# Performance work log

Measured on AMD Instinct MI355X. Metric: run time of the kernel, lower is better.

The kernel has to match this reference:

```python
import jax, jax.numpy as jnp
import numpy as np

N_NODES = 50000
IN_CH = 256
Z_DIM = 64
N_EDGES = 800000


def setup_inputs() -> dict:
    key = jax.random.key(0)
    k_x, k_e, k_wm, k_ws = jax.random.split(key, 4)
    x = jax.random.normal(k_x, (N_NODES, IN_CH), dtype=jnp.float32)
    edge_index = jax.random.randint(k_e, (2, N_EDGES), 0, N_NODES, dtype=jnp.int64)
    # Glorot-style init like PyG GCNConv
    scale = 1.0 / np.sqrt(IN_CH)
    W_mu = jax.random.uniform(k_wm, (IN_CH, Z_DIM), dtype=jnp.float32, minval=-scale, maxval=scale)
    W_logstd = jax.random.uniform(k_ws, (IN_CH, Z_DIM), dtype=jnp.float32, minval=-scale, maxval=scale)
    b_mu = jnp.zeros((Z_DIM,), dtype=jnp.float32)
    b_logstd = jnp.zeros((Z_DIM,), dtype=jnp.float32)
    return {"x": x, "edge_index": edge_index, "W_mu": W_mu, "b_mu": b_mu,
            "W_logstd": W_logstd, "b_logstd": b_logstd}


def _gcn_conv(x, W, b, src, dst, deg_inv_sqrt, num_nodes):
    # PyG GCNConv: out = D^{-1/2} (A + I) D^{-1/2} X W + b
    xw = x @ W                                   # [N, Z]
    norm = deg_inv_sqrt[src] * deg_inv_sqrt[dst]  # [E+N]
    msg = xw[src] * norm[:, None]                 # gather + scale, [E+N, Z]
    agg = jax.ops.segment_sum(msg, dst, num_segments=num_nodes)  # scatter-add
    return agg + b


def reference(x, edge_index, W_mu, b_mu, W_logstd, b_logstd):
    num_nodes = x.shape[0]
    loops = jnp.arange(num_nodes, dtype=edge_index.dtype)
    src = jnp.concatenate([edge_index[0], loops])
    dst = jnp.concatenate([edge_index[1], loops])
    # degree (with self loops) on target nodes, symmetric normalization
    deg = jax.ops.segment_sum(jnp.ones_like(dst, dtype=x.dtype), dst, num_segments=num_nodes)
    deg_inv_sqrt = jnp.where(deg > 0, jax.lax.rsqrt(jnp.maximum(deg, 1.0)), 0.0)
    mu = _gcn_conv(x, W_mu, b_mu, src, dst, deg_inv_sqrt, num_nodes)
    logstd = _gcn_conv(x, W_logstd, b_logstd, src, dst, deg_inv_sqrt, num_nodes)
    return (mu, logstd)
```

## Files before the change

kernel.cpp:

```cpp
#include <hip/hip_runtime.h>

#define N_NODES 50000
#define IN_CH   256
#define Z_DIM   64
#define N_EDGES 800000
#define CH2     128
#define NODE_OFF (N_NODES * Z_DIM)
#define NBLK    ((N_NODES + 255) / 256)
#define SEG     8
#define SEGN    50048
#define NBUCKET (SEG * SEGN)
#define CAP     16
#define CAPN    64
#define ECHUNKS (N_EDGES / 256)
#define TM      128
#define GTILES  ((N_NODES + TM - 1) / TM)
#define NW      32768

typedef __bf16 bf16x8 __attribute__((ext_vector_type(8)));
typedef float  f32x4  __attribute__((ext_vector_type(4)));

__device__ __forceinline__ unsigned short f2bf(float f) {
    __bf16 h = (__bf16)f;
    unsigned short u;
    __builtin_memcpy(&u, &h, 2);
    return u;
}
__device__ __forceinline__ float bf_lo(unsigned w) { return __uint_as_float(w << 16); }
__device__ __forceinline__ float bf_hi(unsigned w) { return __uint_as_float(w & 0xFFFF0000u); }

__global__ void k_pre(int* __restrict__ cur8,
                      const float* __restrict__ Wmu, const float* __restrict__ Wls,
                      unsigned short* __restrict__ WbT) {
    int g = blockIdx.x * 256 + threadIdx.x;
    if (g < NBUCKET) cur8[g] = 0;
    int h = g - NBUCKET;
    if (h >= 0 && h < NW) {
        int n = h >> 8, k = h & 255;
        float v = (n < 64) ? Wmu[(size_t)k * 64 + n] : Wls[(size_t)k * 64 + (n - 64)];
        WbT[(size_t)n * 256 + k] = f2bf(v);
    }
}

__global__ __launch_bounds__(256) void k_scat(const int* __restrict__ src,
                                              const int* __restrict__ dst,
                                              int* __restrict__ cur8,
                                              unsigned short* __restrict__ pk2) {
    int e = blockIdx.x * 256 + threadIdx.x;
    int s = src[e];
    int d = dst[e];
    unsigned xcc;
    asm("s_getreg_b32 %0, hwreg(HW_REG_XCC_ID)" : "=s"(xcc));
    int idx = (int)(xcc & (SEG - 1)) * SEGN + d;
    int pos = __hip_atomic_fetch_add(&cur8[idx], 1, __ATOMIC_RELAXED,
                                     __HIP_MEMORY_SCOPE_WORKGROUP);
    if (pos < CAP) pk2[(size_t)idx * CAP + pos] = (unsigned short)s;
}

#define CSP2 136
__global__ __launch_bounds__(256, 2) void k_gemm(const float* __restrict__ x,
                                                 const unsigned short* __restrict__ WbT,
                                                 unsigned short* __restrict__ xwb) {
    __shared__ __align__(16) unsigned short As[TM * 256];
    const int tid = threadIdx.x;
    const int r0  = blockIdx.x * TM;

    {
        int row_l0 = tid >> 3;
        int cb     = (tid & 7) * 32;
#pragma unroll
        for (int r = 0; r < 4; ++r) {
            int row_l = r * 32 + row_l0;
            int row   = r0 + row_l;
            char* dpb = (char*)As + row_l * 512;
            unsigned cswz = (unsigned)((row_l & 7) << 4);
            if (row < N_NODES) {
                const float4* xp = (const float4*)(x + (size_t)row * IN_CH + cb);
#pragma unroll
                for (int i = 0; i < 4; ++i) {
                    float4 a = xp[2 * i];
                    float4 b = xp[2 * i + 1];
                    uint4 w;
                    w.x = (unsigned)f2bf(a.x) | ((unsigned)f2bf(a.y) << 16);
                    w.y = (unsigned)f2bf(a.z) | ((unsigned)f2bf(a.w) << 16);
                    w.z = (unsigned)f2bf(b.x) | ((unsigned)f2bf(b.y) << 16);
                    w.w = (unsigned)f2bf(b.z) | ((unsigned)f2bf(b.w) << 16);
                    *(uint4*)(dpb + (((unsigned)(cb * 2 + i * 16)) ^ cswz)) = w;
                }
            } else {
                uint4 z = make_uint4(0, 0, 0, 0);
#pragma unroll
                for (int i = 0; i < 4; ++i)
                    *(uint4*)(dpb + (((unsigned)(cb * 2 + i * 16)) ^ cswz)) = z;
            }
        }
    }
    __syncthreads();

    const int wv    = tid >> 6;
    const int lane  = tid & 63;
    const int m     = lane & 15;
    const int q     = lane >> 4;
    const int rbase = wv * 32;

    f32x4 acc[2][8] = {};
    const char* apb0 = (const char*)As + (rbase + m) * 512;
    const char* apb1 = apb0 + 16 * 512;
    const unsigned   sw  = (unsigned)((m & 7) << 4);
    const unsigned short* bp = WbT + (size_t)m * 256 + q * 8;

#pragma unroll
    for (int k0 = 0; k0 < IN_CH; k0 += 32) {
        unsigned off = ((unsigned)(q * 16 + 2 * k0)) ^ sw;
        bf16x8 a0 = *(const bf16x8*)(apb0 + off);
        bf16x8 a1 = *(const bf16x8*)(apb1 + off);
#pragma unroll
        for (int nt = 0; nt < 8; ++nt) {
            bf16x8 bf_ = *(const bf16x8*)(bp + (size_t)nt * 16 * 256 + k0);
            acc[0][nt] = __builtin_amdgcn_mfma_f32_16x16x32_bf16(a0, bf_, acc[0][nt], 0, 0, 0);
            acc[1][nt] = __builtin_amdgcn_mfma_f32_16x16x32_bf16(a1, bf_, acc[1][nt], 0, 0, 0);
        }
    }

    __syncthreads();
    {
        unsigned short* Css = As;
#pragma unroll
        for (int mi = 0; mi < 2; ++mi)
#pragma unroll
            for (int nt = 0; nt < 8; ++nt)
#pragma unroll
                for (int r = 0; r < 4; ++r)
                    Css[(rbase + mi * 16 + q * 4 + r) * CSP2 + nt * 16 + m] =
                        f2bf(acc[mi][nt][r]);
    }
    __syncthreads();
    {
        int row_l = tid >> 2;
        int c0    = (tid & 3) * 32;
#pragma unroll
        for (int rr = 0; rr < 2; ++rr) {
            int rl  = rr * 64 + row_l;
            int row = r0 + rl;
            if (row < N_NODES) {
                const uint4* cp = (const uint4*)(As + rl * CSP2 + c0);
                uint4 w0 = cp[0];
                uint4 w1 = cp[1];
                uint4 w2 = cp[2];
                uint4 w3 = cp[3];
                uint4* op = (uint4*)(xwb + (size_t)row * CH2 + c0);
                op[0] = w0; op[1] = w1; op[2] = w2; op[3] = w3;
            }
        }
    }
}

__global__ void k_dinv(const int* __restrict__ cur8,
                       const unsigned short* __restrict__ pk2,
                       float* __restrict__ dinv,
                       unsigned short* __restrict__ plist,
                       unsigned short* __restrict__ degc) {
    int i = blockIdx.x * 256 + threadIdx.x;
    if (i >= N_NODES) return;
    int traw = 1;
    int c[SEG];
#pragma unroll
    for (int s = 0; s < SEG; ++s) {
        int cs = cur8[s * SEGN + i];
        traw += cs;
        c[s] = (cs > CAP) ? CAP : cs;
    }
    dinv[i] = rsqrtf((float)traw);

    unsigned short* dp = plist + (size_t)i * CAPN;
    int off = 0;
#pragma unroll
    for (int s = 0; s < SEG; ++s) {
        const unsigned short* sp = pk2 + ((size_t)(s * SEGN + i)) * CAP;
        int cc = c[s];
        int lim = CAPN - off;
        if (cc > lim) cc = lim;
        for (int j = 0; j < cc; ++j) dp[off + j] = sp[j];
        off += cc;
    }
    degc[i] = (unsigned short)off;
}

__global__ __launch_bounds__(256) void k_gather(const unsigned short* __restrict__ plist,
                                                const unsigned short* __restrict__ degc,
                                                const unsigned short* __restrict__ xwb,
                                                const float* __restrict__ dinv,
                                                const float* __restrict__ bmu,
                                                const float* __restrict__ bls,
                                                float* __restrict__ out) {
    const int i  = blockIdx.x * 16 + (threadIdx.x >> 4);
    const int cl = threadIdx.x & 15;

    const float di  = dinv[i];
    const int   deg = degc[i];

    float acc[8];
    {
        float sq = di * di;
        uint4 w = *(const uint4*)(xwb + (size_t)i * CH2 + cl * 8);
        acc[0] = bf_lo(w.x) * sq; acc[1] = bf_hi(w.x) * sq;
        acc[2] = bf_lo(w.y) * sq; acc[3] = bf_hi(w.y) * sq;
        acc[4] = bf_lo(w.z) * sq; acc[5] = bf_hi(w.z) * sq;
        acc[6] = bf_lo(w.w) * sq; acc[7] = bf_hi(w.w) * sq;
    }

    const unsigned short* lp = plist + (size_t)i * CAPN;
    for (int j = 0; j < deg; j += 4) {
        uint2 pe = *(const uint2*)(lp + j);
        int s0 = (int)(pe.x & 0xFFFFu);
        int s1 = (int)(pe.x >> 16);
        int s2 = (int)(pe.y & 0xFFFFu);
        int s3 = (int)(pe.y >> 16);
        int rem = deg - j;
        int e1 = (rem > 1) ? s1 : s0;
        int e2 = (rem > 2) ? s2 : s0;
        int e3 = (rem > 3) ? s3 : s0;
        float n0 = di * dinv[s0];
        float n1 = (rem > 1) ? di * dinv[e1] : 0.f;
        float n2 = (rem > 2) ? di * dinv[e2] : 0.f;
        float n3 = (rem > 3) ? di * dinv[e3] : 0.f;
        const uint4 w0 = *(const uint4*)(xwb + (size_t)s0 * CH2 + cl * 8);
        const uint4 w1 = *(const uint4*)(xwb + (size_t)e1 * CH2 + cl * 8);
        const uint4 w2 = *(const uint4*)(xwb + (size_t)e2 * CH2 + cl * 8);
        const uint4 w3 = *(const uint4*)(xwb + (size_t)e3 * CH2 + cl * 8);
        acc[0] += bf_lo(w0.x) * n0 + bf_lo(w1.x) * n1 + bf_lo(w2.x) * n2 + bf_lo(w3.x) * n3;
        acc[1] += bf_hi(w0.x) * n0 + bf_hi(w1.x) * n1 + bf_hi(w2.x) * n2 + bf_hi(w3.x) * n3;
        acc[2] += bf_lo(w0.y) * n0 + bf_lo(w1.y) * n1 + bf_lo(w2.y) * n2 + bf_lo(w3.y) * n3;
        acc[3] += bf_hi(w0.y) * n0 + bf_hi(w1.y) * n1 + bf_hi(w2.y) * n2 + bf_hi(w3.y) * n3;
        acc[4] += bf_lo(w0.z) * n0 + bf_lo(w1.z) * n1 + bf_lo(w2.z) * n2 + bf_lo(w3.z) * n3;
        acc[5] += bf_hi(w0.z) * n0 + bf_hi(w1.z) * n1 + bf_hi(w2.z) * n2 + bf_hi(w3.z) * n3;
        acc[6] += bf_lo(w0.w) * n0 + bf_lo(w1.w) * n1 + bf_lo(w2.w) * n2 + bf_lo(w3.w) * n3;
        acc[7] += bf_hi(w0.w) * n0 + bf_hi(w1.w) * n1 + bf_hi(w2.w) * n2 + bf_hi(w3.w) * n3;
    }

    {
        int c0 = cl * 8;
        const float* bb = (c0 < 64) ? (bmu + c0) : (bls + (c0 - 64));
        float4 b0 = *(const float4*)(bb + 0);
        float4 b1 = *(const float4*)(bb + 4);
        float* o = (c0 < 64) ? (out + (size_t)i * 64 + c0)
                             : (out + NODE_OFF + (size_t)i * 64 + (c0 - 64));
        *(float4*)(o + 0) = make_float4(acc[0] + b0.x, acc[1] + b0.y,
                                        acc[2] + b0.z, acc[3] + b0.w);
        *(float4*)(o + 4) = make_float4(acc[4] + b1.x, acc[5] + b1.y,
                                        acc[6] + b1.z, acc[7] + b1.w);
    }
}

extern "C" void kernel_launch(void* const* d_in, const int* in_sizes, int n_in,
                              void* d_out, int out_size, void* d_ws, size_t ws_size,
                              hipStream_t stream) {
    const float* x   = (const float*)d_in[0];
    const int*   ei  = (const int*)d_in[1];
    const float* Wmu = (const float*)d_in[2];
    const float* bmu = (const float*)d_in[3];
    const float* Wls = (const float*)d_in[4];
    const float* bls = (const float*)d_in[5];
    float* out = (float*)d_out;

    const int* src = ei;
    const int* dst = ei + N_EDGES;

    char* ws = (char*)d_ws;
    int*            cur8  = (int*)(ws + 0);
    float*          dinv  = (float*)(ws + 1638400);
    unsigned short* WbT   = (unsigned short*)(ws + 1867776);
    unsigned short* pk2   = (unsigned short*)(ws + 2097152);
    unsigned short* xwb   = (unsigned short*)(ws + 16777216);
    unsigned short* plist = (unsigned short*)(ws + 29577216);
    unsigned short* degc  = (unsigned short*)(ws + 35977216);

    k_pre<<<(NBUCKET + NW + 255) / 256, 256, 0, stream>>>(cur8, Wmu, Wls, WbT);
    k_scat<<<ECHUNKS, 256, 0, stream>>>(src, dst, cur8, pk2);
    k_gemm<<<GTILES, 256, 0, stream>>>(x, WbT, xwb);
    k_dinv<<<NBLK, 256, 0, stream>>>(cur8, pk2, dinv, plist, degc);
    k_gather<<<N_NODES / 16, 256, 0, stream>>>(plist, degc, xwb, dinv, bmu, bls, out);
}
```

Before: 204.5 us.

## Parallelize per-node bucket compaction across 8 lanes and bucket scatter by block

The degree/compaction kernel now assigns eight lanes per node, one per segment bucket, and uses a segmented shuffle prefix-sum to compute output offsets, so the serial copy of up to 64 entries per thread becomes parallel copies with better coalescing. The edge scatter stops reading the XCC id register and picks the segment from blockIdx instead, switching to device-scope atomicAdd. This is meant to remove the long serial per-thread loop in compaction. In exchange, the atomics now use a wider scope and the blockIdx-based segment no longer tracks the physical die, which may add cross-die atomic contention.

```diff
diff --git a/kernel.cpp b/kernel.cpp
--- a/kernel.cpp
+++ b/kernel.cpp
@@ -6,7 +6,6 @@
 #define N_EDGES 800000
 #define CH2     128
 #define NODE_OFF (N_NODES * Z_DIM)
-#define NBLK    ((N_NODES + 255) / 256)
 #define SEG     8
 #define SEGN    50048
 #define NBUCKET (SEG * SEGN)
@@ -15,6 +14,7 @@
 #define ECHUNKS (N_EDGES / 256)
 #define TM      128
 #define GTILES  ((N_NODES + TM - 1) / TM)
+#define DBLK    ((N_NODES + 31) / 32)
 #define NW      32768
 
 typedef __bf16 bf16x8 __attribute__((ext_vector_type(8)));
@@ -49,11 +49,8 @@
     int e = blockIdx.x * 256 + threadIdx.x;
     int s = src[e];
     int d = dst[e];
-    unsigned xcc;
-    asm("s_getreg_b32 %0, hwreg(HW_REG_XCC_ID)" : "=s"(xcc));
-    int idx = (int)(xcc & (SEG - 1)) * SEGN + d;
-    int pos = __hip_atomic_fetch_add(&cur8[idx], 1, __ATOMIC_RELAXED,
-                                     __HIP_MEMORY_SCOPE_WORKGROUP);
+    int idx = (blockIdx.x & (SEG - 1)) * SEGN + d;
+    int pos = atomicAdd(&cur8[idx], 1);
     if (pos < CAP) pk2[(size_t)idx * CAP + pos] = (unsigned short)s;
 }
 
@@ -155,35 +152,43 @@
     }
 }
 
-__global__ void k_dinv(const int* __restrict__ cur8,
-                       const unsigned short* __restrict__ pk2,
-                       float* __restrict__ dinv,
-                       unsigned short* __restrict__ plist,
-                       unsigned short* __restrict__ degc) {
-    int i = blockIdx.x * 256 + threadIdx.x;
+__global__ __launch_bounds__(256) void k_dinv(const int* __restrict__ cur8,
+                                              const unsigned short* __restrict__ pk2,
+                                              float* __restrict__ dinv,
+                                              unsigned short* __restrict__ plist,
+                                              unsigned short* __restrict__ degc) {
+    const int i = blockIdx.x * 32 + (threadIdx.x >> 3);
+    const int s = threadIdx.x & 7;
     if (i >= N_NODES) return;
-    int traw = 1;
-    int c[SEG];
-#pragma unroll
-    for (int s = 0; s < SEG; ++s) {
-        int cs = cur8[s * SEGN + i];
-        traw += cs;
-        c[s] = (cs > CAP) ? CAP : cs;
-    }
-    dinv[i] = rsqrtf((float)traw);
-
-    unsigned short* dp = plist + (size_t)i * CAPN;
-    int off = 0;
-#pragma unroll
-    for (int s = 0; s < SEG; ++s) {
-        const unsigned short* sp = pk2 + ((size_t)(s * SEGN + i)) * CAP;
-        int cc = c[s];
-        int lim = CAPN - off;
-        if (cc > lim) cc = lim;
-        for (int j = 0; j < cc; ++j) dp[off + j] = sp[j];
-        off += cc;
-    }
-    degc[i] = (unsigned short)off;
+
+    int cnt = cur8[s * SEGN + i];
+    int cc  = (cnt > CAP) ? CAP : cnt;
+
+    int run = cc;
+#pragma unroll
+    for (int k = 1; k < 8; k <<= 1) {
+        int v = __shfl_up(run, k, 8);
+        if (s >= k) run += v;
+    }
+    int tot = cnt;
+#pragma unroll
+    for (int k = 1; k < 8; k <<= 1) tot += __shfl_xor(tot, k, 8);
+
+    int total_c = __shfl(run, 7, 8);
+
+    int off = run - cc;
+    int lim = CAPN - off;
+    if (lim < 0) lim = 0;
+    if (cc > lim) cc = lim;
+
+    const unsigned short* sp = pk2 + ((size_t)(s * SEGN + i)) * CAP;
+    unsigned short*       dp = plist + (size_t)i * CAPN + off;
+    for (int j = 0; j < cc; ++j) dp[j] = sp[j];
+
+    if (s == 0) {
+        dinv[i] = rsqrtf((float)(1 + tot));
+        degc[i] = (unsigned short)((total_c > CAPN) ? CAPN : total_c);
+    }
 }
 
 __global__ __launch_bounds__(256) void k_gather(const unsigned short* __restrict__ plist,
@@ -278,6 +283,6 @@
     k_pre<<<(NBUCKET + NW + 255) / 256, 256, 0, stream>>>(cur8, Wmu, Wls, WbT);
     k_scat<<<ECHUNKS, 256, 0, stream>>>(src, dst, cur8, pk2);
     k_gemm<<<GTILES, 256, 0, stream>>>(x, WbT, xwb);
-    k_dinv<<<NBLK, 256, 0, stream>>>(cur8, pk2, dinv, plist, degc);
+    k_dinv<<<DBLK, 256, 0, stream>>>(cur8, pk2, dinv, plist, degc);
     k_gather<<<N_NODES / 16, 256, 0, stream>>>(plist, degc, xwb, dinv, bmu, bls, out);
 }
```

Measured after the change: 199.6 us. -2.4%, faster.
